# Kernel optimization log

Hardware: AMD Instinct MI355X
Metric: run time of the kernel (lower is better)

The kernel has to match this reference:

```python
import jax, jax.numpy as jnp
import numpy as np

N_NODES = 50000
N_EDGES = 500000
SQRT3_INV = 1.0 / np.sqrt(3.0).astype(np.float32)  # CG norm for 1e x 1e -> 0e
SQRT2_INV = 1.0 / np.sqrt(2.0).astype(np.float32)  # CG norm for 1e x 1e -> 1e


def setup_inputs() -> dict:
    key = jax.random.key(0)
    k1, k2, k3, k4, k5 = jax.random.split(key, 5)
    X = jax.random.normal(k1, (N_NODES, 128), dtype=jnp.float32)   # 32x0e + 32x1e
    Y = jax.random.normal(k2, (N_EDGES, 4), dtype=jnp.float32)     # 0e + 1e (edge SH)
    W = jax.random.normal(k3, (N_EDGES, 160), dtype=jnp.float32)   # 5 paths x 32 mul
    rows = jax.random.randint(k4, (N_EDGES,), 0, N_NODES, dtype=jnp.int64)  # receivers
    cols = jax.random.randint(k5, (N_EDGES,), 0, N_NODES, dtype=jnp.int64)  # senders
    return {"X": X, "Y": Y, "W": W, "rows": rows, "cols": cols}


def _edge_messages(Xj, Y, W):
    # Xj: [E,128] gathered sender features, Y: [E,4], W: [E,160]
    E = Xj.shape[0]
    x0 = Xj[:, :32]                       # [E,32]   32x0e
    x1 = Xj[:, 32:].reshape(E, 32, 3)     # [E,32,3] 32x1e
    y0 = Y[:, 0:1]                        # [E,1]    0e
    y1 = Y[:, 1:4]                        # [E,3]    1e
    w = W.reshape(E, 5, 32)               # per-path uvu weights
    # CG paths (uvu):
    p1 = w[:, 0] * x0 * y0                                     # 0e x 0e -> 0e  [E,32]
    p2 = (w[:, 1] * x0)[:, :, None] * y1[:, None, :]           # 0e x 1e -> 1e  [E,32,3]
    p3 = w[:, 2][:, :, None] * x1 * y0[:, :, None]             # 1e x 0e -> 1e  [E,32,3]
    p4 = w[:, 3] * jnp.einsum('eua,ea->eu', x1, y1) * SQRT3_INV  # 1e x 1e -> 0e [E,32]
    p5 = w[:, 4][:, :, None] * jnp.cross(x1, y1[:, None, :]) * SQRT2_INV  # 1e x 1e -> 1e
    return jnp.concatenate(
        [p1, p2.reshape(E, 96), p3.reshape(E, 96), p4, p5.reshape(E, 96)], axis=1
    )  # [E,352]


def reference(X, Y, W, rows, cols):
    # z_i = sum_{(i,j,e)} W_e (x_j (x)_CG y_e); rows = receiver i, cols = sender j
    Xj = X[cols]                              # per-edge gather [E,128]
    msg = _edge_messages(Xj, Y, W)            # [E,352]
    Z = jax.ops.segment_sum(msg, rows, num_segments=X.shape[0])  # scatter-add
    return Z
```

## Files before the change

kernel.cpp:

```cpp
#include <hip/hip_runtime.h>


#define SQRT3_INV 0.57735026918962576451f
#define SQRT2_INV 0.70710678118654752440f
#define KCAP 64

typedef __attribute__((ext_vector_type(4))) float f4;
typedef __attribute__((ext_vector_type(2))) int   i2;
struct F3 { float a, b, c; };

#define EDGE_BODY(EC_)                                                        \
    do {                                                                      \
        const float* We = W + (size_t)(unsigned)(EC_).x * 160;                \
        const float* Xr = X + (size_t)(unsigned)(EC_).y * 128;                \
        const f4 yv = *reinterpret_cast<const f4*>(Y + (size_t)(unsigned)(EC_).x * 4); \
        const float x0 = Xr[u];                                               \
        const F3 x1 = *reinterpret_cast<const F3*>(Xr + 32 + 3 * u);          \
        const float x1a = x1.a, x1b = x1.b, x1c = x1.c;                       \
        const float y0 = yv.x, y1a = yv.y, y1b = yv.z, y1c = yv.w;            \
        const float w0 = __builtin_nontemporal_load(We + u);                  \
        const float w1 = __builtin_nontemporal_load(We + 32 + u);             \
        const float w2 = __builtin_nontemporal_load(We + 64 + u);             \
        const float w3 = __builtin_nontemporal_load(We + 96 + u);             \
        const float w4 = __builtin_nontemporal_load(We + 128 + u);            \
        a1 += w0 * x0 * y0;                                                   \
        const float w1x0 = w1 * x0;                                           \
        a2a += w1x0 * y1a; a2b += w1x0 * y1b; a2c += w1x0 * y1c;              \
        const float w2y0 = w2 * y0;                                           \
        a3a += w2y0 * x1a; a3b += w2y0 * x1b; a3c += w2y0 * x1c;              \
        const float dot = x1a * y1a + x1b * y1b + x1c * y1c;                  \
        a4 += w3 * dot * SQRT3_INV;                                           \
        const float w4s = w4 * SQRT2_INV;                                     \
        a5a += w4s * (x1b * y1c - x1c * y1b);                                 \
        a5b += w4s * (x1c * y1a - x1a * y1c);                                 \
        a5c += w4s * (x1a * y1b - x1b * y1a);                                 \
    } while (0)

__global__ void scatter_bin_kernel(const int* __restrict__ rows, const int* __restrict__ cols,
                                   int* __restrict__ cnt, i2* __restrict__ slots,
                                   int* __restrict__ ovf_list, int n_nodes, int nE) {
    int e = blockIdx.x * blockDim.x + threadIdx.x;
    if (e >= nE) return;
    int r = rows[e];
    int p = atomicAdd(&cnt[r], 1);
    if (p < KCAP) {
        i2 rec; rec.x = e; rec.y = cols[e];
        slots[(size_t)r * KCAP + p] = rec;
    } else {
        int q = atomicAdd(&cnt[n_nodes], 1);
        ovf_list[q] = e;
    }
}

__global__ __launch_bounds__(256) void tpc_gather(
    const float* __restrict__ X,
    const float* __restrict__ Y,
    const float* __restrict__ W,
    const i2* __restrict__ slots,
    const int* __restrict__ cnt,
    float* __restrict__ Z,
    int n_nodes)
{
    int node = blockIdx.x * 4 + (threadIdx.x >> 6);
    if (node >= n_nodes) return;
    const int lane = threadIdx.x & 63;
    const int u    = lane & 31;
    const int slot = lane >> 5;

    float a1 = 0.f, a2a = 0.f, a2b = 0.f, a2c = 0.f;
    float a3a = 0.f, a3b = 0.f, a3c = 0.f, a4 = 0.f;
    float a5a = 0.f, a5b = 0.f, a5c = 0.f;

    int n = cnt[node];
    if (n > KCAP) n = KCAP;
    const i2* sb = slots + (size_t)node * KCAP;

    int i = 0;
    for (; i + 3 < n; i += 4) {
        const i2 ec0 = sb[i + slot];
        const i2 ec1 = sb[i + 2 + slot];
        EDGE_BODY(ec0);
        EDGE_BODY(ec1);
    }
    for (; i + slot < n; i += 2) {
        const i2 ec0 = sb[i + slot];
        EDGE_BODY(ec0);
    }

    a1  += __shfl_xor(a1,  32, 64);
    a2a += __shfl_xor(a2a, 32, 64);
    a2b += __shfl_xor(a2b, 32, 64);
    a2c += __shfl_xor(a2c, 32, 64);
    a3a += __shfl_xor(a3a, 32, 64);
    a3b += __shfl_xor(a3b, 32, 64);
    a3c += __shfl_xor(a3c, 32, 64);
    a4  += __shfl_xor(a4,  32, 64);
    a5a += __shfl_xor(a5a, 32, 64);
    a5b += __shfl_xor(a5b, 32, 64);
    a5c += __shfl_xor(a5c, 32, 64);

    if (slot == 0) {
        float* Zr = Z + (size_t)node * 352;
        __builtin_nontemporal_store(a1,  Zr + u);
        __builtin_nontemporal_store(a2a, Zr + 32 + 3 * u + 0);
        __builtin_nontemporal_store(a2b, Zr + 32 + 3 * u + 1);
        __builtin_nontemporal_store(a2c, Zr + 32 + 3 * u + 2);
        __builtin_nontemporal_store(a3a, Zr + 128 + 3 * u + 0);
        __builtin_nontemporal_store(a3b, Zr + 128 + 3 * u + 1);
        __builtin_nontemporal_store(a3c, Zr + 128 + 3 * u + 2);
        __builtin_nontemporal_store(a4,  Zr + 224 + u);
        __builtin_nontemporal_store(a5a, Zr + 256 + 3 * u + 0);
        __builtin_nontemporal_store(a5b, Zr + 256 + 3 * u + 1);
        __builtin_nontemporal_store(a5c, Zr + 256 + 3 * u + 2);
    }
}

__global__ void ovf_kernel(const float* __restrict__ X, const float* __restrict__ Y,
                           const float* __restrict__ W, const int* __restrict__ rows,
                           const int* __restrict__ cols, const int* __restrict__ cnt,
                           const int* __restrict__ ovf_list, float* __restrict__ Z,
                           int n_nodes) {
    const int total = cnt[n_nodes] * 32;
    for (int idx = blockIdx.x * blockDim.x + threadIdx.x; idx < total;
         idx += gridDim.x * blockDim.x) {
        const int e = ovf_list[idx >> 5];
        const int u = idx & 31;
        const int r = rows[e];
        const int c = cols[e];
        const float* Xr = X + (size_t)c * 128;
        const float x0 = Xr[u];
        const float x1a = Xr[32 + 3 * u], x1b = Xr[33 + 3 * u], x1c = Xr[34 + 3 * u];
        const float* Ye = Y + (size_t)e * 4;
        const float y0 = Ye[0], y1a = Ye[1], y1b = Ye[2], y1c = Ye[3];
        const float* We = W + (size_t)e * 160;
        const float w0 = We[u], w1 = We[32 + u], w2 = We[64 + u], w3 = We[96 + u], w4 = We[128 + u];
        const float w1x0 = w1 * x0;
        const float w2y0 = w2 * y0;
        const float dot = x1a * y1a + x1b * y1b + x1c * y1c;
        const float w4s = w4 * SQRT2_INV;
        float* Zr = Z + (size_t)r * 352;
        atomicAdd(&Zr[u], w0 * x0 * y0);
        atomicAdd(&Zr[32 + 3 * u + 0], w1x0 * y1a);
        atomicAdd(&Zr[32 + 3 * u + 1], w1x0 * y1b);
        atomicAdd(&Zr[32 + 3 * u + 2], w1x0 * y1c);
        atomicAdd(&Zr[128 + 3 * u + 0], w2y0 * x1a);
        atomicAdd(&Zr[128 + 3 * u + 1], w2y0 * x1b);
        atomicAdd(&Zr[128 + 3 * u + 2], w2y0 * x1c);
        atomicAdd(&Zr[224 + u], w3 * dot * SQRT3_INV);
        atomicAdd(&Zr[256 + 3 * u + 0], w4s * (x1b * y1c - x1c * y1b));
        atomicAdd(&Zr[256 + 3 * u + 1], w4s * (x1c * y1a - x1a * y1c));
        atomicAdd(&Zr[256 + 3 * u + 2], w4s * (x1a * y1b - x1b * y1a));
    }
}

__global__ __launch_bounds__(256) void tpc_edge_kernel(
    const float* __restrict__ X, const float* __restrict__ Y, const float* __restrict__ W,
    const int* __restrict__ rows, const int* __restrict__ cols, float* __restrict__ Z, int n_edges)
{
    int gid = blockIdx.x * blockDim.x + threadIdx.x;
    int e = gid >> 5;
    int u = gid & 31;
    if (e >= n_edges) return;
    const int r = rows[e];
    const int c = cols[e];
    const float* Xr = X + (size_t)c * 128;
    const float x0 = Xr[u];
    const float x1a = Xr[32 + 3 * u], x1b = Xr[33 + 3 * u], x1c = Xr[34 + 3 * u];
    const float* Ye = Y + (size_t)e * 4;
    const float y0 = Ye[0], y1a = Ye[1], y1b = Ye[2], y1c = Ye[3];
    const float* We = W + (size_t)e * 160;
    const float w0 = We[u], w1 = We[32 + u], w2 = We[64 + u], w3 = We[96 + u], w4 = We[128 + u];
    const float w1x0 = w1 * x0;
    const float w2y0 = w2 * y0;
    const float dot = x1a * y1a + x1b * y1b + x1c * y1c;
    const float w4s = w4 * SQRT2_INV;
    float* Zr = Z + (size_t)r * 352;
    atomicAdd(&Zr[u], w0 * x0 * y0);
    atomicAdd(&Zr[32 + 3 * u + 0], w1x0 * y1a);
    atomicAdd(&Zr[32 + 3 * u + 1], w1x0 * y1b);
    atomicAdd(&Zr[32 + 3 * u + 2], w1x0 * y1c);
    atomicAdd(&Zr[128 + 3 * u + 0], w2y0 * x1a);
    atomicAdd(&Zr[128 + 3 * u + 1], w2y0 * x1b);
    atomicAdd(&Zr[128 + 3 * u + 2], w2y0 * x1c);
    atomicAdd(&Zr[224 + u], w3 * dot * SQRT3_INV);
    atomicAdd(&Zr[256 + 3 * u + 0], w4s * (x1b * y1c - x1c * y1b));
    atomicAdd(&Zr[256 + 3 * u + 1], w4s * (x1c * y1a - x1a * y1c));
    atomicAdd(&Zr[256 + 3 * u + 2], w4s * (x1a * y1b - x1b * y1a));
}

extern "C" void kernel_launch(void* const* d_in, const int* in_sizes, int n_in,
                              void* d_out, int out_size, void* d_ws, size_t ws_size,
                              hipStream_t stream) {
    const float* X    = (const float*)d_in[0];
    const float* Y    = (const float*)d_in[1];
    const float* W    = (const float*)d_in[2];
    const int*   rows = (const int*)d_in[3];
    const int*   cols = (const int*)d_in[4];
    float* Z = (float*)d_out;

    const int n_edges = in_sizes[3];
    const int n_nodes = in_sizes[0] / 128;

    size_t slots_bytes = (size_t)n_nodes * KCAP * sizeof(i2);
    size_t need = slots_bytes + (size_t)(n_nodes + 1 + n_edges) * sizeof(int);
    if (ws_size < need) {
        hipMemsetAsync(d_out, 0, (size_t)out_size * sizeof(float), stream);
        const long long threads_total = (long long)n_edges * 32;
        const int grid = (int)((threads_total + 255) / 256);
        tpc_edge_kernel<<<grid, 256, 0, stream>>>(X, Y, W, rows, cols, Z, n_edges);
        return;
    }

    char* base = (char*)d_ws;
    i2*  slots    = (i2*)base;
    int* cnt      = (int*)(base + slots_bytes);
    int* ovf_list = cnt + n_nodes + 1;

    hipMemsetAsync(cnt, 0, (size_t)(n_nodes + 1) * sizeof(int), stream);

    const int gE = (n_edges + 255) / 256;
    scatter_bin_kernel<<<gE, 256, 0, stream>>>(rows, cols, cnt, slots, ovf_list, n_nodes, n_edges);

    const int gG = (n_nodes + 3) / 4;
    tpc_gather<<<gG, 256, 0, stream>>>(X, Y, W, slots, cnt, Z, n_nodes);

    ovf_kernel<<<64, 256, 0, stream>>>(X, Y, W, rows, cols, cnt, ovf_list, Z, n_nodes);
}
```

Before: 138.1 us.

## Fold overflow edges into gather kernel and process two edges per binning thread

```diff
diff --git a/kernel.cpp b/kernel.cpp
--- a/kernel.cpp
+++ b/kernel.cpp
@@ -9,11 +9,11 @@
 typedef __attribute__((ext_vector_type(2))) int   i2;
 struct F3 { float a, b, c; };
 
-#define EDGE_BODY(EC_)                                                        \
+#define EDGE_BODY(E_, C_)                                                     \
     do {                                                                      \
-        const float* We = W + (size_t)(unsigned)(EC_).x * 160;                \
-        const float* Xr = X + (size_t)(unsigned)(EC_).y * 128;                \
-        const f4 yv = *reinterpret_cast<const f4*>(Y + (size_t)(unsigned)(EC_).x * 4); \
+        const float* We = W + (size_t)(unsigned)(E_) * 160;                   \
+        const float* Xr = X + (size_t)(unsigned)(C_) * 128;                   \
+        const f4 yv = *reinterpret_cast<const f4*>(Y + (size_t)(unsigned)(E_) * 4); \
         const float x0 = Xr[u];                                               \
         const F3 x1 = *reinterpret_cast<const F3*>(Xr + 32 + 3 * u);          \
         const float x1a = x1.a, x1b = x1.b, x1c = x1.c;                       \
@@ -39,16 +39,38 @@
 __global__ void scatter_bin_kernel(const int* __restrict__ rows, const int* __restrict__ cols,
                                    int* __restrict__ cnt, i2* __restrict__ slots,
                                    int* __restrict__ ovf_list, int n_nodes, int nE) {
-    int e = blockIdx.x * blockDim.x + threadIdx.x;
-    if (e >= nE) return;
-    int r = rows[e];
-    int p = atomicAdd(&cnt[r], 1);
-    if (p < KCAP) {
-        i2 rec; rec.x = e; rec.y = cols[e];
-        slots[(size_t)r * KCAP + p] = rec;
+    int t = blockIdx.x * blockDim.x + threadIdx.x;
+    int e0 = t * 2;
+    if (e0 >= nE) return;
+    if (e0 + 1 < nE) {
+        const i2 rr = *reinterpret_cast<const i2*>(rows + e0);
+        const i2 cc = *reinterpret_cast<const i2*>(cols + e0);
+        int p0 = atomicAdd(&cnt[rr.x], 1);
+        int p1 = atomicAdd(&cnt[rr.y], 1);
+        if (p0 < KCAP) {
+            i2 rec; rec.x = e0; rec.y = cc.x;
+            slots[(size_t)rr.x * KCAP + p0] = rec;
+        } else {
+            int q = atomicAdd(&cnt[n_nodes], 1);
+            ovf_list[q] = e0;
+        }
+        if (p1 < KCAP) {
+            i2 rec; rec.x = e0 + 1; rec.y = cc.y;
+            slots[(size_t)rr.y * KCAP + p1] = rec;
+        } else {
+            int q = atomicAdd(&cnt[n_nodes], 1);
+            ovf_list[q] = e0 + 1;
+        }
     } else {
-        int q = atomicAdd(&cnt[n_nodes], 1);
-        ovf_list[q] = e;
+        int r = rows[e0];
+        int p = atomicAdd(&cnt[r], 1);
+        if (p < KCAP) {
+            i2 rec; rec.x = e0; rec.y = cols[e0];
+            slots[(size_t)r * KCAP + p] = rec;
+        } else {
+            int q = atomicAdd(&cnt[n_nodes], 1);
+            ovf_list[q] = e0;
+        }
     }
 }
 
@@ -56,8 +78,11 @@
     const float* __restrict__ X,
     const float* __restrict__ Y,
     const float* __restrict__ W,
+    const int* __restrict__ rows,
+    const int* __restrict__ cols,
     const i2* __restrict__ slots,
     const int* __restrict__ cnt,
+    const int* __restrict__ ovf_list,
     float* __restrict__ Z,
     int n_nodes)
 {
@@ -71,20 +96,31 @@
     float a3a = 0.f, a3b = 0.f, a3c = 0.f, a4 = 0.f;
     float a5a = 0.f, a5b = 0.f, a5c = 0.f;
 
-    int n = cnt[node];
-    if (n > KCAP) n = KCAP;
+    const int ncnt = cnt[node];
+    int n = ncnt > KCAP ? KCAP : ncnt;
     const i2* sb = slots + (size_t)node * KCAP;
 
     int i = 0;
     for (; i + 3 < n; i += 4) {
         const i2 ec0 = sb[i + slot];
         const i2 ec1 = sb[i + 2 + slot];
-        EDGE_BODY(ec0);
-        EDGE_BODY(ec1);
+        EDGE_BODY(ec0.x, ec0.y);
+        EDGE_BODY(ec1.x, ec1.y);
     }
     for (; i + slot < n; i += 2) {
         const i2 ec0 = sb[i + slot];
-        EDGE_BODY(ec0);
+        EDGE_BODY(ec0.x, ec0.y);
+    }
+
+    if (ncnt > KCAP) {
+        const int tot = cnt[n_nodes];
+        for (int j = slot; j < tot; j += 2) {
+            const int e = ovf_list[j];
+            if (rows[e] == node) {
+                const int c = cols[e];
+                EDGE_BODY(e, c);
+            }
+        }
     }
 
     a1  += __shfl_xor(a1,  32, 64);
@@ -112,44 +148,6 @@
         __builtin_nontemporal_store(a5a, Zr + 256 + 3 * u + 0);
         __builtin_nontemporal_store(a5b, Zr + 256 + 3 * u + 1);
         __builtin_nontemporal_store(a5c, Zr + 256 + 3 * u + 2);
-    }
-}
-
-__global__ void ovf_kernel(const float* __restrict__ X, const float* __restrict__ Y,
-                           const float* __restrict__ W, const int* __restrict__ rows,
-                           const int* __restrict__ cols, const int* __restrict__ cnt,
-                           const int* __restrict__ ovf_list, float* __restrict__ Z,
-                           int n_nodes) {
-    const int total = cnt[n_nodes] * 32;
-    for (int idx = blockIdx.x * blockDim.x + threadIdx.x; idx < total;
-         idx += gridDim.x * blockDim.x) {
-        const int e = ovf_list[idx >> 5];
-        const int u = idx & 31;
-        const int r = rows[e];
-        const int c = cols[e];
-        const float* Xr = X + (size_t)c * 128;
-        const float x0 = Xr[u];
-        const float x1a = Xr[32 + 3 * u], x1b = Xr[33 + 3 * u], x1c = Xr[34 + 3 * u];
-        const float* Ye = Y + (size_t)e * 4;
-        const float y0 = Ye[0], y1a = Ye[1], y1b = Ye[2], y1c = Ye[3];
-        const float* We = W + (size_t)e * 160;
-        const float w0 = We[u], w1 = We[32 + u], w2 = We[64 + u], w3 = We[96 + u], w4 = We[128 + u];
-        const float w1x0 = w1 * x0;
-        const float w2y0 = w2 * y0;
-        const float dot = x1a * y1a + x1b * y1b + x1c * y1c;
-        const float w4s = w4 * SQRT2_INV;
-        float* Zr = Z + (size_t)r * 352;
-        atomicAdd(&Zr[u], w0 * x0 * y0);
-        atomicAdd(&Zr[32 + 3 * u + 0], w1x0 * y1a);
-        atomicAdd(&Zr[32 + 3 * u + 1], w1x0 * y1b);
-        atomicAdd(&Zr[32 + 3 * u + 2], w1x0 * y1c);
-        atomicAdd(&Zr[128 + 3 * u + 0], w2y0 * x1a);
-        atomicAdd(&Zr[128 + 3 * u + 1], w2y0 * x1b);
-        atomicAdd(&Zr[128 + 3 * u + 2], w2y0 * x1c);
-        atomicAdd(&Zr[224 + u], w3 * dot * SQRT3_INV);
-        atomicAdd(&Zr[256 + 3 * u + 0], w4s * (x1b * y1c - x1c * y1b));
-        atomicAdd(&Zr[256 + 3 * u + 1], w4s * (x1c * y1a - x1a * y1c));
-        atomicAdd(&Zr[256 + 3 * u + 2], w4s * (x1a * y1b - x1b * y1a));
     }
 }
 
@@ -218,11 +216,10 @@
 
     hipMemsetAsync(cnt, 0, (size_t)(n_nodes + 1) * sizeof(int), stream);
 
-    const int gE = (n_edges + 255) / 256;
+    const int nPairs = (n_edges + 1) / 2;
+    const int gE = (nPairs + 255) / 256;
     scatter_bin_kernel<<<gE, 256, 0, stream>>>(rows, cols, cnt, slots, ovf_list, n_nodes, n_edges);
 
     const int gG = (n_nodes + 3) / 4;
-    tpc_gather<<<gG, 256, 0, stream>>>(X, Y, W, slots, cnt, Z, n_nodes);
-
-    ovf_kernel<<<64, 256, 0, stream>>>(X, Y, W, rows, cols, cnt, ovf_list, Z, n_nodes);
-}
+    tpc_gather<<<gG, 256, 0, stream>>>(X, Y, W, rows, cols, slots, cnt, ovf_list, Z, n_nodes);
+}
```

Result: faster. 134.0 us, median of 2 (-3.0%).
